# Kernel tuning notes

Hardware: AMD Instinct MI355X
Metric: run time of the kernel (lower is better)

## Reference

```python
import jax, jax.numpy as jnp
import numpy as np

B, S, D, H = 128, 512, 256, 256


def _lstm_cell(Wih, Whh, b, x_t, h, c):
    # PyTorch LSTM gate order: i, f, g, o. b = b_ih + b_hh (mathematically equivalent).
    z = x_t @ Wih.T + h @ Whh.T + b  # [B, 4H]
    i, f, g, o = jnp.split(z, 4, axis=-1)
    i = jax.nn.sigmoid(i)
    f = jax.nn.sigmoid(f)
    g = jnp.tanh(g)
    o = jax.nn.sigmoid(o)
    c = f * c + i * g
    h = o * jnp.tanh(c)
    return h, c


def setup_inputs() -> dict:
    key = jax.random.key(0)
    ks = jax.random.split(key, 12)
    s = 1.0 / np.sqrt(H)
    f32 = jnp.float32
    return {
        "x": jax.random.normal(ks[0], (B, S, D), f32),
        "enc_Wih": jax.random.uniform(ks[1], (4 * H, D), f32, -s, s),
        "enc_Whh": jax.random.uniform(ks[2], (4 * H, H), f32, -s, s),
        "enc_b": jax.random.uniform(ks[3], (4 * H,), f32, -s, s),
        "dec_Wih": jax.random.uniform(ks[4], (4 * H, D), f32, -s, s),
        "dec_Whh": jax.random.uniform(ks[5], (4 * H, H), f32, -s, s),
        "dec_b": jax.random.uniform(ks[6], (4 * H,), f32, -s, s),
        "W1_w": jax.random.uniform(ks[7], (H, H), f32, -s, s),
        "W1_b": jax.random.uniform(ks[8], (H,), f32, -s, s),
        "W2_w": jax.random.uniform(ks[9], (H, H), f32, -s, s),
        "W2_b": jax.random.uniform(ks[10], (H,), f32, -s, s),
        "vt_w": jax.random.uniform(ks[11], (H,), f32, -s, s),
    }


def reference(x, enc_Wih, enc_Whh, enc_b, dec_Wih, dec_Whh, dec_b,
              W1_w, W1_b, W2_w, W2_b, vt_w):
    b_, s_, d_ = x.shape
    h0 = jnp.zeros((b_, H), x.dtype)
    c0 = jnp.zeros((b_, H), x.dtype)

    # ---- encoder LSTM over time ----
    def enc_step(carry, x_t):
        h, c = carry
        h, c = _lstm_cell(enc_Wih, enc_Whh, enc_b, x_t, h, c)
        return (h, c), h

    (h, c), enc_out = jax.lax.scan(enc_step, (h0, c0), jnp.swapaxes(x, 0, 1))
    enc_out = jnp.swapaxes(enc_out, 0, 1)  # [B, S, H]

    # W1(encoder_outputs) is loop-invariant; compute once (same math as original)
    enc_proj = enc_out @ W1_w.T + W1_b  # [B, S, H]

    # ---- pointer decode loop ----
    def dec_step(carry, _):
        h, c, din = carry
        h, c = _lstm_cell(dec_Wih, dec_Whh, dec_b, din, h, c)
        q = h @ W2_w.T + W2_b  # [B, H]
        u = jnp.einsum('bsh,h->bs', jnp.tanh(enc_proj + q[:, None, :]), vt_w)
        probs = jax.nn.softmax(u, axis=1)  # [B, S]
        din = jnp.einsum('bs,bsh->bh', probs, enc_out)
        return (h, c, din), probs

    din0 = jnp.zeros((b_, d_), x.dtype)
    _, probs_seq = jax.lax.scan(dec_step, (h, c, din0), None, length=s_)
    return jnp.swapaxes(probs_seq, 0, 1)  # [B, S, S]
```

## Files before the change

kernel.cpp:

```cpp
#include <hip/hip_runtime.h>
#include <hip/hip_fp16.h>

typedef _Float16 h2_t __attribute__((ext_vector_type(2)));
typedef unsigned int u32x4 __attribute__((ext_vector_type(4)));

#define KEXP 2.8853900817779268f

#define BARRIER() do { \
    asm volatile("s_waitcnt lgkmcnt(0)" ::: "memory"); \
    __builtin_amdgcn_s_barrier(); \
    asm volatile("" ::: "memory"); \
} while (0)

__device__ __forceinline__ float fdot2(unsigned int a, unsigned int b, float c) {
#if __has_builtin(__builtin_amdgcn_fdot2)
    return __builtin_amdgcn_fdot2(__builtin_bit_cast(h2_t, a), __builtin_bit_cast(h2_t, b), c, false);
#else
    h2_t ha = __builtin_bit_cast(h2_t, a), hb = __builtin_bit_cast(h2_t, b);
    return c + (float)ha[0]*(float)hb[0] + (float)ha[1]*(float)hb[1];
#endif
}

__device__ __forceinline__ float dot4(u32x4 a, u32x4 b, float c) {
    c = fdot2(a[0], b[0], c); c = fdot2(a[1], b[1], c);
    c = fdot2(a[2], b[2], c); c = fdot2(a[3], b[3], c);
    return c;
}

__device__ __forceinline__ unsigned int pk16(float a, float b) {
    auto h = __builtin_amdgcn_cvt_pkrtz(a, b);
    return __builtin_bit_cast(unsigned int, h);
}

__device__ __forceinline__ float rcp_(float x) {
#if __has_builtin(__builtin_amdgcn_rcpf)
    return __builtin_amdgcn_rcpf(x);
#else
    return 1.0f / x;
#endif
}

__device__ __forceinline__ float sigm(float x) { return rcp_(1.0f + __expf(-x)); }
__device__ __forceinline__ float tanh_(float x) {
    float e = __expf(2.0f * x);
    return 1.0f - 2.0f * rcp_(e + 1.0f);
}

__device__ __forceinline__ unsigned int rcp1p2exp(unsigned int s) {
    __half2 e = h2exp2(__builtin_bit_cast(__half2, s));
    __half2 d = __hadd2(e, __float2half2_rn(1.0f));
    return __builtin_bit_cast(unsigned int, h2rcp(d));
}
__device__ __forceinline__ unsigned int hadd2u(unsigned int a, unsigned int b) {
    return __builtin_bit_cast(unsigned int,
        __hadd2(__builtin_bit_cast(__half2, a), __builtin_bit_cast(__half2, b)));
}

__device__ __forceinline__ void st_u32(unsigned int* p, unsigned int v) {
    __hip_atomic_store(p, v, __ATOMIC_RELAXED, __HIP_MEMORY_SCOPE_AGENT);
}
__device__ __forceinline__ unsigned int ld_u32(const unsigned int* p) {
    return __hip_atomic_load(p, __ATOMIC_RELAXED, __HIP_MEMORY_SCOPE_AGENT);
}
__device__ __forceinline__ float ld_f32(const unsigned int* p) {
    return __builtin_bit_cast(float, ld_u32(p));
}
__device__ __forceinline__ float h2f_lo(unsigned int v) {
    return __half2float(__ushort_as_half((unsigned short)(v & 0xffffu)));
}
__device__ __forceinline__ float h2f_hi(unsigned int v) {
    return __half2float(__ushort_as_half((unsigned short)(v >> 16)));
}

__global__ void init_flags_kernel(unsigned int* flags) {
    flags[threadIdx.x * 32] = 0u;
}

__global__ __launch_bounds__(256) void prep_kernel(
    const float* __restrict__ encWhh, const float* __restrict__ decWih,
    const float* __restrict__ decWhh, const float* __restrict__ W2w,
    u32x4* __restrict__ We8, u32x4* __restrict__ Wi8, u32x4* __restrict__ Wh8, u32x4* __restrict__ W28)
{
    int id = blockIdx.x * 256 + threadIdx.x;
    if (id < 3 * 32768) {
        int mat = id >> 15, local = id & 32767;
        int j = local & 1023, k8 = local >> 10;
        const float* src = mat == 0 ? encWhh : (mat == 1 ? decWih : decWhh);
        u32x4* dst = mat == 0 ? We8 : (mat == 1 ? Wi8 : Wh8);
        const float* p = src + (size_t)j * 256 + k8 * 8;
        float4 a = *(const float4*)p; float4 c = *(const float4*)(p + 4);
        u32x4 v; v[0] = pk16(a.x, a.y); v[1] = pk16(a.z, a.w);
        v[2] = pk16(c.x, c.y); v[3] = pk16(c.z, c.w);
        dst[k8 * 1024 + j] = v;
    } else {
        int local = id - 3 * 32768;
        if (local < 8192) {
            int m = local & 255, k8 = local >> 8;
            const float* p = W2w + (size_t)m * 256 + k8 * 8;
            float4 a = *(const float4*)p; float4 c = *(const float4*)(p + 4);
            u32x4 v; v[0] = pk16(a.x, a.y); v[1] = pk16(a.z, a.w);
            v[2] = pk16(c.x, c.y); v[3] = pk16(c.z, c.w);
            W28[k8 * 256 + m] = v;
        }
    }
}

template<int A_IS_F16, int TR_OUT>
__global__ __launch_bounds__(256) void gemm_kernel(
    const void* __restrict__ A_, const float* __restrict__ Bw,
    const float* __restrict__ bias, unsigned short* __restrict__ C, int N, float scale)
{
    __shared__ float As[16][68];
    __shared__ float Bs[16][132];
    const int t = threadIdx.x;
    const int row0 = blockIdx.y * 64, col0 = blockIdx.x * 128;
    const int ty = t >> 4, tx = t & 15;
    const int lm = t & 63, lkq = t >> 6;
    const int ln = t & 127, lkq2 = t >> 7;
    float acc[4][8] = {};
    for (int k0 = 0; k0 < 256; k0 += 16) {
        float4 av;
        if constexpr (A_IS_F16) {
            const unsigned short* A = (const unsigned short*)A_;
            uint2 ha = *(const uint2*)(A + (size_t)(row0 + lm) * 256 + k0 + lkq * 4);
            h2_t h0 = __builtin_bit_cast(h2_t, ha.x);
            h2_t h1 = __builtin_bit_cast(h2_t, ha.y);
            av = make_float4((float)h0[0], (float)h0[1], (float)h1[0], (float)h1[1]);
        } else {
            av = *(const float4*)((const float*)A_ + (size_t)(row0 + lm) * 256 + k0 + lkq * 4);
        }
        const float* bp = Bw + (size_t)(col0 + ln) * 256 + k0 + lkq2 * 8;
        float4 bv0 = *(const float4*)bp;
        float4 bv1 = *(const float4*)(bp + 4);
        __syncthreads();
        As[lkq * 4 + 0][lm] = av.x;
        As[lkq * 4 + 1][lm] = av.y;
        As[lkq * 4 + 2][lm] = av.z;
        As[lkq * 4 + 3][lm] = av.w;
        Bs[lkq2 * 8 + 0][ln] = bv0.x;
        Bs[lkq2 * 8 + 1][ln] = bv0.y;
        Bs[lkq2 * 8 + 2][ln] = bv0.z;
        Bs[lkq2 * 8 + 3][ln] = bv0.w;
        Bs[lkq2 * 8 + 4][ln] = bv1.x;
        Bs[lkq2 * 8 + 5][ln] = bv1.y;
        Bs[lkq2 * 8 + 6][ln] = bv1.z;
        Bs[lkq2 * 8 + 7][ln] = bv1.w;
        __syncthreads();
        #pragma unroll
        for (int kk = 0; kk < 16; ++kk) {
            float4 a = *(float4*)&As[kk][ty * 4];
            float4 b0 = *(float4*)&Bs[kk][tx * 8];
            float4 b1 = *(float4*)&Bs[kk][tx * 8 + 4];
            float ar[4] = {a.x, a.y, a.z, a.w};
            float br[8] = {b0.x, b0.y, b0.z, b0.w, b1.x, b1.y, b1.z, b1.w};
            #pragma unroll
            for (int i = 0; i < 4; ++i)
                #pragma unroll
                for (int j = 0; j < 8; ++j)
                    acc[i][j] = fmaf(ar[i], br[j], acc[i][j]);
        }
    }
    float bv[8];
    #pragma unroll
    for (int j = 0; j < 8; ++j) bv[j] = bias[col0 + tx * 8 + j];
    #pragma unroll
    for (int i = 0; i < 4; ++i) {
        unsigned int w0 = pk16((acc[i][0] + bv[0]) * scale, (acc[i][1] + bv[1]) * scale);
        unsigned int w1 = pk16((acc[i][2] + bv[2]) * scale, (acc[i][3] + bv[3]) * scale);
        unsigned int w2 = pk16((acc[i][4] + bv[4]) * scale, (acc[i][5] + bv[5]) * scale);
        unsigned int w3 = pk16((acc[i][6] + bv[6]) * scale, (acc[i][7] + bv[7]) * scale);
        uint4 val = make_uint4(w0, w1, w2, w3);
        if constexpr (TR_OUT) {
            int rr = row0 + ty * 4 + i;
            int bb = rr >> 9, s = rr & 511;
            int c8 = (col0 >> 3) + tx;
            ((uint4*)C)[(size_t)bb * 16384 + (size_t)c8 * 512 + s] = val;
        } else {
            *(uint4*)(C + (size_t)(row0 + ty * 4 + i) * N + col0 + tx * 8) = val;
        }
    }
}

__global__ __launch_bounds__(1024) void encoder_kernel(
    const unsigned short* __restrict__ Xproj, const u32x4* __restrict__ We8,
    float* __restrict__ hfin, float* __restrict__ cfin,
    unsigned short* __restrict__ enc_h, unsigned int* __restrict__ encT,
    unsigned int* __restrict__ xh, unsigned int* __restrict__ eflags)
{
    const int blk = blockIdx.x;
    const int b = blk & 127, r = blk >> 7;
    const int t = threadIdx.x;
    __shared__ __align__(16) float zs[1024];
    __shared__ __align__(16) unsigned int hh2[128];
    if (t < 128) hh2[t] = 0u;
    float c_reg = 0.f;
    unsigned int hprev_u = 0u;
    __syncthreads();

    const int jl = t & 511, kh = t >> 9;
    const int rowA = ((jl >> 7) << 8) + r * 128 + (jl & 127);
    const u32x4* wp = We8 + (size_t)(kh * 16) * 1024 + rowA;
    const unsigned short* xp = Xproj + (size_t)b * 524288 + rowA;
    const int fo_me = (b * 2 + r) * 32, fo_pr = (b * 2 + (1 - r)) * 32;
    unsigned int* xh_me = xh + (b * 2 + r) * 512;
    const unsigned int* xh_pr = xh + (b * 2 + (1 - r)) * 512;

    for (int step = 0; step < 512; ++step) {
        float acc = (kh == 0)
            ? __half2float(__ushort_as_half(__builtin_nontemporal_load(xp + (size_t)step * 1024)))
            : 0.f;
        #pragma unroll 8
        for (int i = 0; i < 16; ++i) {
            u32x4 wv = wp[i * 1024];
            u32x4 hv = *(const u32x4*)&hh2[(kh * 16 + i) * 4];
            acc = dot4(wv, hv, acc);
        }
        zs[t] = acc;
        BARRIER();
        if (t < 128) {
            float gi = sigm(zs[t] + zs[t + 512]);
            float gf = sigm(zs[128 + t] + zs[640 + t]);
            float gg = tanh_(zs[256 + t] + zs[768 + t]);
            float go_ = sigm(zs[384 + t] + zs[896 + t]);
            c_reg = gf * c_reg + gi * gg;
            float h = go_ * tanh_(c_reg);
            float hnb = __shfl_down(h, 1);
            if (!(t & 1)) {
                unsigned int hp = pk16(h, hnb);
                hh2[r * 64 + (t >> 1)] = hp;
                st_u32(&xh_me[t >> 1], hp);
            }
            asm volatile("s_waitcnt vmcnt(0)" ::: "memory");
        }
        BARRIER();
        if (t == 0) {
            unsigned int T = (unsigned)(step + 1);
            st_u32(&eflags[fo_me], T);
            while (ld_u32(&eflags[fo_pr]) < T) __builtin_amdgcn_s_sleep(1);
        }
        BARRIER();
        if (t < 64) hh2[(1 - r) * 64 + t] = ld_u32(&xh_pr[t]);
        BARRIER();
        if (t < 256) {
            unsigned int hp = hh2[t >> 1];
            unsigned int hv16 = (t & 1) ? (hp >> 16) : (hp & 0xffffu);
            if (r == 0) {
                __builtin_nontemporal_store((unsigned short)hv16,
                                            enc_h + (size_t)(b * 512 + step) * 256 + t);
            } else {
                if (step & 1) {
                    int s2 = step >> 1;
                    encT[(size_t)b * 65536 + (size_t)((s2 >> 2) * 256 + t) * 4 + (s2 & 3)] =
                        hprev_u | (hv16 << 16);
                }
                hprev_u = hv16;
            }
        }
        BARRIER();
    }
    if (t < 128) {
        unsigned int hp = hh2[r * 64 + (t >> 1)];
        float hv = (t & 1) ? h2f_hi(hp) : h2f_lo(hp);
        hfin[b * 256 + r * 128 + t] = hv;
        cfin[b * 256 + r * 128 + t] = c_reg;
    }
}

__global__ __launch_bounds__(1024) void decoder_kernel(
    const u32x4* __restrict__ Wi8, const u32x4* __restrict__ Wh8, const u32x4* __restrict__ W28,
    const float* __restrict__ dec_b, const float* __restrict__ W2b, const float* __restrict__ vtw,
    const float* __restrict__ hfin, const float* __restrict__ cfin,
    const u32x4* __restrict__ projT, const u32x4* __restrict__ encT,
    unsigned int* __restrict__ xgate, unsigned int* __restrict__ xdin,
    unsigned int* __restrict__ xsum, unsigned int* __restrict__ flags,
    float* __restrict__ out)
{
    const int blk = blockIdx.x;
    const int b = blk & 127, r = blk >> 7;
    const int t = threadIdx.x;
    const int lane = t & 63, w = t >> 6;

    __shared__ __align__(16) float zs[1024];
    __shared__ __align__(16) unsigned int hh2[128];
    __shared__ __align__(16) unsigned int din2[128];
    __shared__ __align__(16) unsigned int qp2[128];
    __shared__ __align__(16) unsigned int mv2u[128];
    __shared__ __align__(16) unsigned int p2u[128];
    __shared__ float wreds[16];
    __shared__ float svtS, rsS;

    const int fo_me = (b * 2 + r) * 32, fo_pr = (b * 2 + (1 - r)) * 32;
    const int go_me = (b * 2 + r) * 256, go_pr = (b * 2 + (1 - r)) * 256;

    float c_reg = (t < 128) ? cfin[b * 256 + r * 128 + t] : 0.f;
    const float w2b_r = (t < 256) ? W2b[t] : 0.f;
    if (t < 128) { din2[t] = 0u; mv2u[t] = pk16(-2.f * vtw[2 * t], -2.f * vtw[2 * t + 1]); }
    if (t < 256) zs[t] = vtw[t];
    __syncthreads();
    if (t < 64) {
        float v = zs[t] + zs[t + 64] + zs[t + 128] + zs[t + 192];
        #pragma unroll
        for (int off = 1; off < 64; off <<= 1) v += __shfl_xor(v, off);
        if (t == 0) svtS = v;
    }
    if (t < 256) {
        float h0 = hfin[b * 256 + t];
        float hnb = __shfl_down(h0, 1);
        if (!(t & 1)) hh2[t >> 1] = pk16(h0, hnb);
    }
    __syncthreads();
    const float svt = svtS;

    const int jl = t & 511, kh = t >> 9;
    const int rowA = ((jl >> 7) << 8) + r * 128 + (jl & 127);
    const float bseed = (kh == 0) ? dec_b[rowA] : 0.f;
    const u32x4* wpi = Wi8 + rowA;
    const u32x4* wph = Wh8 + rowA;
    const int hF = t & 255, slF = t >> 8;
    const int sl4 = t >> 2, qr = t & 3;
    const int s_g = r * 256 + sl4;
    const u32x4* pD = projT + (size_t)b * 16384 + (size_t)(qr * 8) * 512 + s_g;
    const u32x4* fD = encT + (size_t)b * 16384 + (size_t)(r * 32 + slF * 8) * 256 + hF;
    float* outp = out + (size_t)b * 262144;

    for (int step = 0; step < 512; ++step) {
        float acc = bseed;
        #pragma unroll 8
        for (int k8 = 0; k8 < 16; ++k8) {
            u32x4 wv = wpi[(kh * 16 + k8) * 1024];
            u32x4 dv = *(const u32x4*)&din2[(kh * 16 + k8) * 4];
            acc = dot4(wv, dv, acc);
        }
        #pragma unroll 8
        for (int k8 = 0; k8 < 16; ++k8) {
            u32x4 wv = wph[(kh * 16 + k8) * 1024];
            u32x4 hv = *(const u32x4*)&hh2[(kh * 16 + k8) * 4];
            acc = dot4(wv, hv, acc);
        }
        zs[t] = acc;
        BARRIER();
        if (t < 128) {
            float gi = sigm(zs[t] + zs[t + 512]);
            float gf = sigm(zs[128 + t] + zs[640 + t]);
            float gg = tanh_(zs[256 + t] + zs[768 + t]);
            float go_ = sigm(zs[384 + t] + zs[896 + t]);
            c_reg = gf * c_reg + gi * gg;
            float h = go_ * tanh_(c_reg);
            float hnb = __shfl_down(h, 1);
            if (!(t & 1)) {
                unsigned int hp = pk16(h, hnb);
                hh2[r * 64 + (t >> 1)] = hp;
                st_u32(&xgate[go_me + (t >> 1)], hp);
            }
            asm volatile("s_waitcnt vmcnt(0)" ::: "memory");
        }
        BARRIER();
        if (t == 0) {
            unsigned int T = (unsigned)(2 * step + 1);
            st_u32(&flags[fo_me], T);
            while (ld_u32(&flags[fo_pr]) < T) __builtin_amdgcn_s_sleep(1);
        }
        BARRIER();
        if (t < 64) hh2[(1 - r) * 64 + t] = ld_u32(&xgate[go_pr + t]);
        BARRIER();
        {
            float qa = 0.f;
            #pragma unroll
            for (int i = 0; i < 8; ++i) {
                int k8 = slF * 8 + i;
                u32x4 wv = W28[k8 * 256 + hF];
                u32x4 hv = *(const u32x4*)&hh2[k8 * 4];
                qa = dot4(wv, hv, qa);
            }
            zs[t] = qa;
        }
        BARRIER();
        if (t < 256) {
            float q = (w2b_r + zs[t] + zs[t + 256] + zs[t + 512] + zs[t + 768]) * KEXP;
            float qnx = __shfl_down(q, 1);
            if (!(t & 1)) qp2[t >> 1] = pk16(q, qnx);
        }
        BARRIER();
        float e;
        u32x4 fv[8];
        {
            float up = 0.f;
            #pragma unroll 4
            for (int i = 0; i < 8; ++i) {
                u32x4 pv = pD[i * 512];
                int c = qr * 8 + i;
                u32x4 qh = *(const u32x4*)&qp2[c * 4];
                u32x4 mv = *(const u32x4*)&mv2u[c * 4];
                up = fdot2(mv[0], rcp1p2exp(hadd2u(pv[0], qh[0])), up);
                up = fdot2(mv[1], rcp1p2exp(hadd2u(pv[1], qh[1])), up);
                up = fdot2(mv[2], rcp1p2exp(hadd2u(pv[2], qh[2])), up);
                up = fdot2(mv[3], rcp1p2exp(hadd2u(pv[3], qh[3])), up);
            }
            up += __shfl_xor(up, 1);
            up += __shfl_xor(up, 2);
            e = __expf(up + svt);
            #pragma unroll
            for (int j = 0; j < 8; ++j) fv[j] = fD[j * 256];
            float enx = __shfl_down(e, 4);
            if (!(t & 7)) p2u[t >> 3] = pk16(e, enx);
            float ws = e;
            #pragma unroll
            for (int off = 1; off < 64; off <<= 1) ws += __shfl_xor(ws, off);
            if (lane == 0) wreds[w] = ws;
        }
        BARRIER();
        {
            float fa = 0.f;
            #pragma unroll
            for (int j = 0; j < 8; ++j) {
                u32x4 ev = fv[j];
                u32x4 pw = *(const u32x4*)&p2u[(slF * 8 + j) * 4];
                fa = dot4(ev, pw, fa);
            }
            zs[t] = fa;
        }
        BARRIER();
        float dpart = 0.f;
        if (t < 256) {
            dpart = zs[t] + zs[t + 256] + zs[t + 512] + zs[t + 768];
            st_u32(&xdin[go_me + t], __builtin_bit_cast(unsigned int, dpart));
            asm volatile("s_waitcnt vmcnt(0)" ::: "memory");
        }
        BARRIER();
        if (t == 0) {
            float ls = 0.f;
            #pragma unroll
            for (int k = 0; k < 16; ++k) ls += wreds[k];
            ls *= 0.25f;
            st_u32(&xsum[fo_me], __builtin_bit_cast(unsigned int, ls));
            asm volatile("s_waitcnt vmcnt(0)" ::: "memory");
            unsigned int T = (unsigned)(2 * step + 2);
            st_u32(&flags[fo_me], T);
            while (ld_u32(&flags[fo_pr]) < T) __builtin_amdgcn_s_sleep(1);
            float lr = __builtin_bit_cast(float, ld_u32(&xsum[fo_pr]));
            rsS = rcp_(ls + lr);
        }
        BARRIER();
        {
            float rs = rsS;
            if (t < 256) {
                float drem = __builtin_bit_cast(float, ld_u32(&xdin[go_pr + t]));
                float dval = (dpart + drem) * rs;
                float dnx = __shfl_down(dval, 1);
                if (!(t & 1)) din2[t >> 1] = pk16(dval, dnx);
            }
            if ((t & 3) == 0) outp[(size_t)step * 512 + s_g] = e * rs;
        }
        BARRIER();
    }
}

extern "C" void kernel_launch(void* const* d_in, const int* in_sizes, int n_in,
                              void* d_out, int out_size, void* d_ws, size_t ws_size,
                              hipStream_t stream) {
    const float* x      = (const float*)d_in[0];
    const float* encWih = (const float*)d_in[1];
    const float* encWhh = (const float*)d_in[2];
    const float* enc_b  = (const float*)d_in[3];
    const float* decWih = (const float*)d_in[4];
    const float* decWhh = (const float*)d_in[5];
    const float* dec_bp = (const float*)d_in[6];
    const float* W1w    = (const float*)d_in[7];
    const float* W1b    = (const float*)d_in[8];
    const float* W2w    = (const float*)d_in[9];
    const float* W2bp   = (const float*)d_in[10];
    const float* vtw    = (const float*)d_in[11];

    char* ws = (char*)d_ws;
    u32x4* We8 = (u32x4*)(ws);
    u32x4* Wi8 = (u32x4*)(ws + 524288);
    u32x4* Wh8 = (u32x4*)(ws + 1048576);
    u32x4* W28 = (u32x4*)(ws + 1572864);
    unsigned short* enc_h = (unsigned short*)(ws + 1703936);
    unsigned int*   encT  = (unsigned int*)(ws + 35258368);
    unsigned short* projT = (unsigned short*)(ws + 68812800);
    float* hfin = (float*)(ws + 102367232);
    float* cfin = (float*)(ws + 102498304);

    unsigned int* flags = (unsigned int*)(ws + 1703936);
    unsigned int* xsum  = (unsigned int*)(ws + 1703936 + 32768);
    unsigned int* xgate = (unsigned int*)(ws + 1703936 + 65536);
    unsigned int* xdin  = (unsigned int*)(ws + 1703936 + 65536 + 262144);

    unsigned int* eflags = (unsigned int*)(ws + 68812800);
    unsigned int* exh    = (unsigned int*)(ws + 68812800 + 32768);

    unsigned short* Xproj = (unsigned short*)d_out;

    prep_kernel<<<416, 256, 0, stream>>>(encWhh, decWih, decWhh, W2w, We8, Wi8, Wh8, W28);
    gemm_kernel<0, 0><<<dim3(8, 1024), 256, 0, stream>>>(x, encWih, enc_b, Xproj, 1024, 1.0f);
    init_flags_kernel<<<1, 256, 0, stream>>>(eflags);
    encoder_kernel<<<256, 1024, 0, stream>>>(Xproj, We8, hfin, cfin, enc_h, (unsigned int*)encT,
                                             exh, eflags);
    gemm_kernel<1, 1><<<dim3(2, 1024), 256, 0, stream>>>(enc_h, W1w, W1b, projT, 256, KEXP);
    init_flags_kernel<<<1, 256, 0, stream>>>(flags);
    decoder_kernel<<<256, 1024, 0, stream>>>(Wi8, Wh8, W28, dec_bp, W2bp, vtw,
                                             hfin, cfin, (const u32x4*)projT, (const u32x4*)encT,
                                             xgate, xdin, xsum, flags, (float*)d_out);
}
```

Baseline: 13.64 ms.

## Cut block barriers in LSTM loops with per-thread flag polling and shuffle reductions

Every thread now polls the partner block's flag itself, instead of thread 0 polling and then a block barrier. This removes one barrier per cross-block handshake in both the encoder and decoder loops. The W2 query matvec and the attention-weighted context sum are remapped so partial sums are combined with wavefront shuffles rather than a shared-memory stage plus barrier. The softmax normaliser is computed redundantly by every thread instead of being broadcast through shared memory. The trade-off is many more threads spinning on global flags and some redundant arithmetic, in exchange for a shorter chain of serial synchronisation points on the critical path.

Measured after the change: 16.69 ms. +22.4%, slower.

```diff
diff --git a/kernel.cpp b/kernel.cpp
--- a/kernel.cpp
+++ b/kernel.cpp
@@ -233,12 +233,11 @@
             asm volatile("s_waitcnt vmcnt(0)" ::: "memory");
         }
         BARRIER();
-        if (t == 0) {
+        {
             unsigned int T = (unsigned)(step + 1);
-            st_u32(&eflags[fo_me], T);
+            if (t == 0) st_u32(&eflags[fo_me], T);
             while (ld_u32(&eflags[fo_pr]) < T) __builtin_amdgcn_s_sleep(1);
         }
-        BARRIER();
         if (t < 64) hh2[(1 - r) * 64 + t] = ld_u32(&xh_pr[t]);
         BARRIER();
         if (t < 256) {
@@ -287,13 +286,13 @@
     __shared__ __align__(16) unsigned int mv2u[128];
     __shared__ __align__(16) unsigned int p2u[128];
     __shared__ float wreds[16];
-    __shared__ float svtS, rsS;
+    __shared__ float svtS;
 
     const int fo_me = (b * 2 + r) * 32, fo_pr = (b * 2 + (1 - r)) * 32;
     const int go_me = (b * 2 + r) * 256, go_pr = (b * 2 + (1 - r)) * 256;
 
     float c_reg = (t < 128) ? cfin[b * 256 + r * 128 + t] : 0.f;
-    const float w2b_r = (t < 256) ? W2b[t] : 0.f;
+    const float w2b_s = (t < 512 && !(t & 1)) ? W2b[t >> 1] : 0.f;
     if (t < 128) { din2[t] = 0u; mv2u[t] = pk16(-2.f * vtw[2 * t], -2.f * vtw[2 * t + 1]); }
     if (t < 256) zs[t] = vtw[t];
     __syncthreads();
@@ -316,11 +315,12 @@
     const float bseed = (kh == 0) ? dec_b[rowA] : 0.f;
     const u32x4* wpi = Wi8 + rowA;
     const u32x4* wph = Wh8 + rowA;
-    const int hF = t & 255, slF = t >> 8;
+    const int hq = t >> 1, kh2 = t & 1;
     const int sl4 = t >> 2, qr = t & 3;
     const int s_g = r * 256 + sl4;
     const u32x4* pD = projT + (size_t)b * 16384 + (size_t)(qr * 8) * 512 + s_g;
-    const u32x4* fD = encT + (size_t)b * 16384 + (size_t)(r * 32 + slF * 8) * 256 + hF;
+    const int hN = t >> 2, qc = t & 3;
+    const u32x4* fD = encT + (size_t)b * 16384 + (size_t)(r * 32 + qc * 8) * 256 + hN;
     float* outp = out + (size_t)b * 262144;
 
     for (int step = 0; step < 512; ++step) {
@@ -355,30 +355,26 @@
             asm volatile("s_waitcnt vmcnt(0)" ::: "memory");
         }
         BARRIER();
-        if (t == 0) {
+        {
             unsigned int T = (unsigned)(2 * step + 1);
-            st_u32(&flags[fo_me], T);
+            if (t == 0) st_u32(&flags[fo_me], T);
             while (ld_u32(&flags[fo_pr]) < T) __builtin_amdgcn_s_sleep(1);
         }
-        BARRIER();
         if (t < 64) hh2[(1 - r) * 64 + t] = ld_u32(&xgate[go_pr + t]);
         BARRIER();
-        {
-            float qa = 0.f;
+        if (t < 512) {
+            float qa = w2b_s;
             #pragma unroll
-            for (int i = 0; i < 8; ++i) {
-                int k8 = slF * 8 + i;
-                u32x4 wv = W28[k8 * 256 + hF];
+            for (int i = 0; i < 16; ++i) {
+                int k8 = kh2 * 16 + i;
+                u32x4 wv = W28[k8 * 256 + hq];
                 u32x4 hv = *(const u32x4*)&hh2[k8 * 4];
                 qa = dot4(wv, hv, qa);
             }
-            zs[t] = qa;
-        }
-        BARRIER();
-        if (t < 256) {
-            float q = (w2b_r + zs[t] + zs[t + 256] + zs[t + 512] + zs[t + 768]) * KEXP;
-            float qnx = __shfl_down(q, 1);
-            if (!(t & 1)) qp2[t >> 1] = pk16(q, qnx);
+            qa += __shfl_xor(qa, 1);
+            float q = qa * KEXP;
+            float qnx = __shfl_down(q, 2);
+            if (!(t & 3)) qp2[t >> 2] = pk16(q, qnx);
         }
         BARRIER();
         float e;
@@ -414,42 +410,42 @@
             #pragma unroll
             for (int j = 0; j < 8; ++j) {
                 u32x4 ev = fv[j];
-                u32x4 pw = *(const u32x4*)&p2u[(slF * 8 + j) * 4];
+                u32x4 pw = *(const u32x4*)&p2u[(qc * 8 + j) * 4];
                 fa = dot4(ev, pw, fa);
             }
-            zs[t] = fa;
-        }
-        BARRIER();
-        float dpart = 0.f;
-        if (t < 256) {
-            dpart = zs[t] + zs[t + 256] + zs[t + 512] + zs[t + 768];
-            st_u32(&xdin[go_me + t], __builtin_bit_cast(unsigned int, dpart));
+            fa += __shfl_xor(fa, 1);
+            fa += __shfl_xor(fa, 2);
+            if (!(t & 3)) {
+                zs[hN] = fa;
+                st_u32(&xdin[go_me + hN], __builtin_bit_cast(unsigned int, fa));
+            }
             asm volatile("s_waitcnt vmcnt(0)" ::: "memory");
         }
         BARRIER();
-        if (t == 0) {
+        {
+            unsigned int T = (unsigned)(2 * step + 2);
+            if (t == 0) {
+                float ls = 0.f;
+                #pragma unroll
+                for (int k = 0; k < 16; ++k) ls += wreds[k];
+                st_u32(&xsum[fo_me], __builtin_bit_cast(unsigned int, ls * 0.25f));
+                asm volatile("s_waitcnt vmcnt(0)" ::: "memory");
+                st_u32(&flags[fo_me], T);
+            }
+            while (ld_u32(&flags[fo_pr]) < T) __builtin_amdgcn_s_sleep(1);
+        }
+        {
             float ls = 0.f;
             #pragma unroll
             for (int k = 0; k < 16; ++k) ls += wreds[k];
-            ls *= 0.25f;
-            st_u32(&xsum[fo_me], __builtin_bit_cast(unsigned int, ls));
-            asm volatile("s_waitcnt vmcnt(0)" ::: "memory");
-            unsigned int T = (unsigned)(2 * step + 2);
-            st_u32(&flags[fo_me], T);
-            while (ld_u32(&flags[fo_pr]) < T) __builtin_amdgcn_s_sleep(1);
-            float lr = __builtin_bit_cast(float, ld_u32(&xsum[fo_pr]));
-            rsS = rcp_(ls + lr);
-        }
-        BARRIER();
-        {
-            float rs = rsS;
+            float lr = ld_f32(&xsum[fo_pr]);
+            float rs = rcp_(ls * 0.25f + lr);
             if (t < 256) {
-                float drem = __builtin_bit_cast(float, ld_u32(&xdin[go_pr + t]));
-                float dval = (dpart + drem) * rs;
+                float dval = (zs[t] + ld_f32(&xdin[go_pr + t])) * rs;
                 float dnx = __shfl_down(dval, 1);
                 if (!(t & 1)) din2[t >> 1] = pk16(dval, dnx);
             }
-            if ((t & 3) == 0) outp[(size_t)step * 512 + s_g] = e * rs;
+            if (!(t & 3)) outp[(size_t)step * 512 + s_g] = e * rs;
         }
         BARRIER();
     }
```
